# Kernel tuning notes

Hardware: AMD Instinct MI355X
Metric: run time of the kernel (lower is better)

Reference implementation:

```python
import jax, jax.numpy as jnp
import numpy as np

EPS = 1e-5  # BatchNorm eps


def _conv3x3(x, w, b):
    # x: [B,C,H,W], w: [O,C,3,3], b: [O]
    y = jax.lax.conv_general_dilated(
        x, w, window_strides=(1, 1), padding=((1, 1), (1, 1)),
        dimension_numbers=("NCHW", "OIHW", "NCHW"))
    return y + b[None, :, None, None]


def _bilinear_gather(x, py, px):
    """Bilinear sample x at fractional coords (zero outside bounds).
    x: [B,C,H,W]; py, px: [B,K,H,W] -> returns [B,C,K,H,W]."""
    B, C, H, W = x.shape
    K = py.shape[1]
    x_flat = x.reshape(B, C, H * W)
    y0 = jnp.floor(py)
    x0 = jnp.floor(px)
    wy1 = py - y0
    wx1 = px - x0
    wy0 = 1.0 - wy1
    wx0 = 1.0 - wx1

    def gather(yi, xi):
        valid = (yi >= 0) & (yi <= H - 1) & (xi >= 0) & (xi <= W - 1)
        yc = jnp.clip(yi, 0, H - 1).astype(jnp.int32)
        xc = jnp.clip(xi, 0, W - 1).astype(jnp.int32)
        idx = (yc * W + xc).reshape(B, 1, K * H * W)
        g = jnp.take_along_axis(x_flat, idx, axis=2).reshape(B, C, K, H, W)
        return g * valid.astype(x.dtype)[:, None]

    val = (gather(y0, x0) * (wy0 * wx0)[:, None]
           + gather(y0, x0 + 1.0) * (wy0 * wx1)[:, None]
           + gather(y0 + 1.0, x0) * (wy1 * wx0)[:, None]
           + gather(y0 + 1.0, x0 + 1.0) * (wy1 * wx1)[:, None])
    return val


def _deform_conv_bn_relu(x, w_off, b_off, w_dcn, b_dcn, gamma, beta):
    B, Ci, H, W = x.shape
    Co = w_dcn.shape[0]
    # offset/mask branch: 27 = 9 dy | 9 dx (cat, then interpreted interleaved) | 9 mask
    om = _conv3x3(x, w_off, b_off)                       # [B,27,H,W]
    offset = jnp.concatenate([om[:, :9], om[:, 9:18]], axis=1)  # [B,18,H,W]
    mask = jax.nn.sigmoid(om[:, 18:27])                  # [B,9,H,W]
    dy = offset[:, 0::2]                                 # [B,9,H,W]
    dx = offset[:, 1::2]                                 # [B,9,H,W]
    # base sampling grid: stride 1, pad 1, dilation 1, 3x3 kernel
    ky = jnp.repeat(jnp.arange(3, dtype=x.dtype), 3)     # [9]
    kx = jnp.tile(jnp.arange(3, dtype=x.dtype), 3)       # [9]
    hh = jnp.arange(H, dtype=x.dtype)
    ww = jnp.arange(W, dtype=x.dtype)
    py = dy + (hh - 1.0)[None, None, :, None] + ky[None, :, None, None]
    px = dx + (ww - 1.0)[None, None, None, :] + kx[None, :, None, None]
    sampled = _bilinear_gather(x, py, px)                # [B,Ci,9,H,W]
    sampled = sampled * mask[:, None]                    # modulated (DCNv2)
    out = jnp.einsum('bckhw,ock->bohw', sampled, w_dcn.reshape(Co, Ci, 9))
    out = out + b_dcn[None, :, None, None]
    # BatchNorm2d (training mode: batch statistics, biased variance) + ReLU
    mean = jnp.mean(out, axis=(0, 2, 3), keepdims=True)
    var = jnp.mean(jnp.square(out - mean), axis=(0, 2, 3), keepdims=True)
    bn = (out - mean) * jax.lax.rsqrt(var + EPS)
    bn = bn * gamma[None, :, None, None] + beta[None, :, None, None]
    return jax.nn.relu(bn)


def setup_inputs() -> dict:
    key = jax.random.key(0)
    k0, k1, k2 = jax.random.split(key, 3)
    B, Ci, Co, H, W = 2, 256, 256, 96, 96
    x = jax.random.normal(k0, (B, Ci, H, W), jnp.float32)
    # small offset-conv weights -> offsets within a few pixels (realistic after training)
    w_off = jax.random.normal(k1, (27, Ci, 3, 3), jnp.float32) * 0.01
    b_off = jnp.zeros((27,), jnp.float32)
    w_dcn = jax.random.normal(k2, (Co, Ci, 3, 3), jnp.float32) * (1.0 / np.sqrt(Ci * 9))
    b_dcn = jnp.zeros((Co,), jnp.float32)
    gamma = jnp.ones((Co,), jnp.float32)
    beta = jnp.zeros((Co,), jnp.float32)
    return {"x": x, "w_off": w_off, "b_off": b_off, "w_dcn": w_dcn,
            "b_dcn": b_dcn, "gamma": gamma, "beta": beta}


def reference(x, w_off, b_off, w_dcn, b_dcn, gamma, beta):
    return _deform_conv_bn_relu(x, w_off, b_off, w_dcn, b_dcn, gamma, beta)
```

## Files before the change

### kernel.cpp

```cpp
#include <hip/hip_runtime.h>


typedef unsigned short ushort_t;
typedef unsigned int uint_t;
typedef __attribute__((ext_vector_type(8))) short bf16x8;
typedef __attribute__((ext_vector_type(4))) float f32x4;
typedef __attribute__((ext_vector_type(2))) float f32x2v;

#define HH 96
#define WW 96
#define HWSZ 9216
#define CI 256
#define CO 256
#define NB 2
#define NPIX 18432
#define KTOT 2304

__device__ __forceinline__ ushort_t f2bf(float f) {
  unsigned int u = __float_as_uint(f);
  u += 0x7fffu + ((u >> 16) & 1u);
  return (ushort_t)(u >> 16);
}
__device__ __forceinline__ float u2f(uint_t u) { return __uint_as_float(u); }

__device__ __forceinline__ void gload16(const void* g, void* l) {
  __builtin_amdgcn_global_load_lds(
      (const __attribute__((address_space(1))) unsigned int*)g,
      (__attribute__((address_space(3))) unsigned int*)l, 16, 0, 0);
}

__global__ void cvt_w9(const float* __restrict__ w, ushort_t* __restrict__ o) {
  int i = blockIdx.x * 256 + threadIdx.x;
  int oo = i / KTOT;
  int kk = i - oo * KTOT;
  o[(kk >> 3) * 2048 + oo * 8 + (kk & 7)] = f2bf(w[i]);
}

__global__ void cvt_woff9(const float* __restrict__ w, ushort_t* __restrict__ o) {
  int i = blockIdx.x * 256 + threadIdx.x;
  int m = i / KTOT;
  int kk = i - m * KTOT;
  float v = (m < 27) ? w[m * KTOT + kk] : 0.f;
  o[(kk >> 3) * 256 + m * 8 + (kk & 7)] = f2bf(v);
}

__global__ __launch_bounds__(512, 2) void off_gemm(
    const float* __restrict__ x, const ushort_t* __restrict__ w27r,
    float* __restrict__ om_part) {
  __shared__ __align__(16) ushort_t A27[2][2048];
  __shared__ __align__(16) ushort_t B64[4096];
  __shared__ uint2 tbl[9][64];

  const int tid = threadIdx.x;
  const int lane = tid & 63, wid = tid >> 6;
  const int p0 = blockIdx.x * 64;
  const int part = blockIdx.y;
  const int bimg = p0 / HWSZ;
  const int hw0 = p0 - bimg * HWSZ;
  const float* xb = x + (size_t)bimg * CI * HWSZ;

  for (int e = tid; e < 576; e += 512) {
    int k = e >> 6, px = e & 63;
    int hw = hw0 + px, h = hw / WW, w_ = hw - h * WW;
    int dy = k / 3 - 1, dx = k % 3 - 1;
    bool ok = (h + dy >= 0) && (h + dy < HH) && (w_ + dx >= 0) && (w_ + dx < WW);
    tbl[k][px] = make_uint2(ok ? (uint_t)(hw + dy * WW + dx) : 0u,
                            ok ? 0x3f800000u : 0u);
  }

  const int lg = lane >> 4, lm = lane & 15;
  const int wr = wid >> 2, wc = wid & 3;
  f32x4 acc = (f32x4){0.f, 0.f, 0.f, 0.f};

  int cj[8], kj[8];
#pragma unroll
  for (int j = 0; j < 8; ++j) {
    int kk = part * 1152 + wid * 8 + j;
    cj[j] = kk / 9;
    kj[j] = kk - 9 * cj[j];
  }
  __syncthreads();

  float rv0[8], rm0[8], rv1[8], rm1[8];
  const int k0 = part * 18;

#define OG_RAW(RV, RM)                                                        \
  { _Pragma("unroll") for (int j = 0; j < 8; ++j) {                           \
      uint2 e_ = tbl[kj[j]][lane];                                            \
      RV[j] = xb[cj[j] * HWSZ + (int)e_.x];                                   \
      RM[j] = u2f(e_.y);                                                      \
      kj[j] += 1; cj[j] += 7;                                                 \
      if (kj[j] == 9) { kj[j] = 0; cj[j] += 1; } } }
#define OG_GA(CH, BUF)                                                        \
  gload16(w27r + (size_t)(CH) * 2048 + (tid & 255) * 8, &A27[BUF][(wid & 3) * 512]);
#define OG_STEP(CUR, RVC, RMC, RVN, RMN, KO)                                  \
  {                                                                           \
    if ((KO) < 17) {                                                          \
      OG_RAW(RVN, RMN)                                                        \
      OG_GA(k0 + (KO) + 1, (CUR) ^ 1)                                         \
      asm volatile("s_waitcnt vmcnt(10)" ::: "memory");                       \
    } else {                                                                  \
      asm volatile("s_waitcnt vmcnt(1)" ::: "memory");                        \
    }                                                                         \
    __builtin_amdgcn_sched_barrier(0);                                        \
    {                                                                         \
      ushort_t sv_[8] __attribute__((aligned(16)));                           \
      _Pragma("unroll") for (int j = 0; j < 8; ++j)                           \
        sv_[j] = f2bf(RVC[j] * RMC[j]);                                       \
      *(uint4*)&B64[tid * 8] = *(const uint4*)sv_;                            \
    }                                                                         \
    if ((KO) < 17) asm volatile("s_waitcnt vmcnt(9) lgkmcnt(0)" ::: "memory"); \
    else           asm volatile("s_waitcnt vmcnt(0) lgkmcnt(0)" ::: "memory"); \
    __builtin_amdgcn_s_barrier();                                             \
    __builtin_amdgcn_sched_barrier(0);                                        \
    _Pragma("unroll") for (int s = 0; s < 2; ++s) {                           \
      bf16x8 af = *(const bf16x8*)&A27[CUR][((s * 4 + lg) * 32 + wr * 16 + lm) * 8]; \
      bf16x8 bfv = *(const bf16x8*)&B64[((s * 4 + lg) * 64 + wc * 16 + lm) * 8];     \
      acc = __builtin_amdgcn_mfma_f32_16x16x32_bf16(af, bfv, acc, 0, 0, 0);   \
    }                                                                         \
    asm volatile("s_waitcnt lgkmcnt(0)" ::: "memory");                        \
    __builtin_amdgcn_s_barrier();                                             \
    __builtin_amdgcn_sched_barrier(0);                                        \
  }

  OG_RAW(rv0, rm0)
  OG_GA(k0, 0)
  for (int ko2 = 0; ko2 < 9; ++ko2) {
    const int ko = ko2 * 2;
    OG_STEP(0, rv0, rm0, rv1, rm1, ko)
    OG_STEP(1, rv1, rm1, rv0, rm0, ko + 1)
  }
#undef OG_RAW
#undef OG_GA
#undef OG_STEP

  int row = wr * 16 + lg * 4;
  int col = p0 + wc * 16 + lm;
#pragma unroll
  for (int r = 0; r < 4; ++r)
    if (row + r < 27)
      om_part[((size_t)(part * 27 + row + r)) * NPIX + col] = acc[r];
}

__global__ void prep_kernel(const float* __restrict__ om_part, const float* __restrict__ b_off,
                            uint_t* __restrict__ offs, float4* __restrict__ wts) {
  int n = blockIdx.x * 128 + threadIdx.x;
  float omv[27];
#pragma unroll
  for (int ch = 0; ch < 27; ++ch)
    omv[ch] = b_off[ch] + om_part[(size_t)ch * NPIX + n] +
              om_part[((size_t)(27 + ch)) * NPIX + n];
  int hw = n % HWSZ;
  int h = hw / WW, w = hw - h * WW;
#pragma unroll
  for (int k = 0; k < 9; ++k) {
    float dy = omv[2 * k], dx = omv[2 * k + 1];
    float mk = 1.f / (1.f + __expf(-omv[18 + k]));
    float py = dy + (float)(h - 1 + k / 3);
    float px = dx + (float)(w - 1 + k % 3);
    float y0f = floorf(py), x0f = floorf(px);
    int y0 = (int)y0f, x0 = (int)x0f;
    float wy1 = py - y0f, wx1 = px - x0f;
    float wy0 = 1.f - wy1, wx0 = 1.f - wx1;
    float vy0 = (y0 >= 0 && y0 <= HH - 1) ? 1.f : 0.f;
    float vy1 = (y0 + 1 >= 0 && y0 + 1 <= HH - 1) ? 1.f : 0.f;
    int yc0 = min(max(y0, 0), HH - 1), yc1 = min(max(y0 + 1, 0), HH - 1);
    int xa = min(max(x0, 0), WW - 2);
    float a_, b_;
    if (x0 >= 0 && x0 <= WW - 2)      { a_ = wx0; b_ = wx1; }
    else if (x0 == -1)                { a_ = wx1; b_ = 0.f; }
    else if (x0 == WW - 1)            { a_ = 0.f; b_ = wx0; }
    else                              { a_ = 0.f; b_ = 0.f; }
    float s0 = mk * vy0 * wy0, s1 = mk * vy1 * wy1;
    offs[(size_t)k * NPIX + n] = (uint_t)(yc0 * WW + xa) | ((uint_t)(yc1 * WW + xa) << 16);
    wts[(size_t)k * NPIX + n] = make_float4(a_ * s0, b_ * s0, a_ * s1, b_ * s1);
  }
}

__global__ __launch_bounds__(512, 2) void sample_lds(
    const float* __restrict__ x, const uint_t* __restrict__ offs,
    const float4* __restrict__ wts, ushort_t* __restrict__ S_g) {
  __shared__ __align__(8) uint_t xp[HWSZ];
  const int tid = threadIdx.x;
  const int img = blockIdx.x >> 1;
  const int half = blockIdx.x & 1;
  const int cp = blockIdx.y;
  const int n0 = img * HWSZ + half * 4608;

  {
    const float* s0 = x + ((size_t)(img * CI + 2 * cp)) * HWSZ;
    const float* s1 = s0 + HWSZ;
#pragma unroll
    for (int i = 0; i < 9; ++i) {
      int col = i * 1024 + tid * 2;
      f32x2v c0 = *(const f32x2v*)(s0 + col);
      f32x2v c1 = *(const f32x2v*)(s1 + col);
      uint2 pk;
      pk.x = (uint_t)f2bf(c0[0]) | ((uint_t)f2bf(c1[0]) << 16);
      pk.y = (uint_t)f2bf(c0[1]) | ((uint_t)f2bf(c1[1]) << 16);
      *(uint2*)&xp[col] = pk;
    }
  }
  __syncthreads();

  for (int j = 0; j < 9; ++j) {
    const int n = n0 + tid + j * 512;
    uint_t ofr[9]; float4 wtr[9];
#pragma unroll
    for (int k = 0; k < 9; ++k) {
      ofr[k] = offs[(size_t)k * NPIX + n];
      wtr[k] = wts[(size_t)k * NPIX + n];
    }
    uint_t pkw[9];
#pragma unroll
    for (int i = 0; i < 9; ++i) pkw[i] = 0u;
#pragma unroll
    for (int k = 0; k < 9; ++k) {
      const int o0 = (int)(ofr[k] & 0xffffu);
      const int o1 = (int)(ofr[k] >> 16);
      uint_t a0 = xp[o0], a1 = xp[o0 + 1];
      uint_t b0 = xp[o1], b1 = xp[o1 + 1];
      float v0 = wtr[k].x * u2f(a0 << 16) + wtr[k].y * u2f(a1 << 16) +
                 wtr[k].z * u2f(b0 << 16) + wtr[k].w * u2f(b1 << 16);
      float v1 = wtr[k].x * u2f(a0 & 0xffff0000u) + wtr[k].y * u2f(a1 & 0xffff0000u) +
                 wtr[k].z * u2f(b0 & 0xffff0000u) + wtr[k].w * u2f(b1 & 0xffff0000u);
      const int q0 = k, q1 = 9 + k;
      pkw[q0 >> 1] |= ((uint_t)f2bf(v0)) << ((q0 & 1) * 16);
      pkw[q1 >> 1] |= ((uint_t)f2bf(v1)) << ((q1 & 1) * 16);
    }
#pragma unroll
    for (int jj = 0; jj < 9; ++jj) {
      const int kk = cp * 18 + 2 * jj;
      *(uint_t*)&S_g[((size_t)(kk >> 3) * NPIX + n) * 8 + (kk & 7)] = pkw[jj];
    }
  }
}

__global__ __launch_bounds__(512, 2) void s_gemm(
    const ushort_t* __restrict__ w9r, const ushort_t* __restrict__ S_g,
    const float* __restrict__ b_dcn, float* __restrict__ out,
    float2* __restrict__ bnp2) {
  __shared__ __align__(16) ushort_t A[4][4096];
  __shared__ __align__(16) ushort_t S[4][4096];

  const int tid = threadIdx.x;
  const int lane = tid & 63, wid = tid >> 6;
  const int p0 = blockIdx.x * 128;
  const int m0 = blockIdx.y * 128;
  const int bimg = p0 / HWSZ;
  const int hw0 = p0 - bimg * HWSZ;
  const int lg = lane >> 4, lm = lane & 15;
  const int wr = wid >> 1, wc = wid & 1;
  const int sg = tid >> 7, sp = tid & 127;

  f32x4 acc[2][4];
#pragma unroll
  for (int i = 0; i < 2; ++i)
#pragma unroll
    for (int j = 0; j < 4; ++j) acc[i][j] = (f32x4){0.f, 0.f, 0.f, 0.f};

#define SG_STAGE(CH, BUF)                                                     \
  {                                                                           \
    gload16(w9r + ((size_t)((CH) * 4 + sg) * 256 + m0 + sp) * 8,              \
            &A[BUF][(sg * 128 + sp) * 8]);                                    \
    gload16(S_g + ((size_t)((CH) * 4 + sg) * NPIX + p0 + sp) * 8,             \
            &S[BUF][(sg * 128 + sp) * 8]);                                    \
  }
#define SG_MFMA(BUF)                                                         \
  {                                                                          \
    bf16x8 af0 = *(const bf16x8*)&A[BUF][(lg * 128 + wr * 32 + lm) * 8];     \
    bf16x8 af1 = *(const bf16x8*)&A[BUF][(lg * 128 + wr * 32 + 16 + lm) * 8];\
    _Pragma("unroll") for (int ni = 0; ni < 4; ++ni) {                       \
      bf16x8 bfv = *(const bf16x8*)&S[BUF][(lg * 128 + wc * 64 + ni * 16 + lm) * 8]; \
      acc[0][ni] = __builtin_amdgcn_mfma_f32_16x16x32_bf16(af0, bfv, acc[0][ni], 0, 0, 0); \
      acc[1][ni] = __builtin_amdgcn_mfma_f32_16x16x32_bf16(af1, bfv, acc[1][ni], 0, 0, 0); \
    }                                                                        \
  }

  SG_STAGE(0, 0)
  SG_STAGE(1, 1)
  for (int ko = 0; ko < 72; ++ko) {
    if (ko < 70) {
      SG_STAGE(ko + 2, (ko + 2) & 3)
      asm volatile("s_waitcnt vmcnt(4)" ::: "memory");
    } else if (ko == 70) {
      asm volatile("s_waitcnt vmcnt(2)" ::: "memory");
    } else {
      asm volatile("s_waitcnt vmcnt(0)" ::: "memory");
    }
    __builtin_amdgcn_s_barrier();
    __builtin_amdgcn_sched_barrier(0);
    SG_MFMA(ko & 3)
  }
#undef SG_STAGE
#undef SG_MFMA

  float bsum[8], bsq[8];
#pragma unroll
  for (int mi = 0; mi < 2; ++mi) {
#pragma unroll
    for (int r = 0; r < 4; ++r) {
      int o = m0 + wr * 32 + mi * 16 + lg * 4 + r;
      float b = b_dcn[o];
      float s = 0.f, q = 0.f;
#pragma unroll
      for (int ni = 0; ni < 4; ++ni) {
        float v = acc[mi][ni][r] + b;
        out[((size_t)(bimg * CO + o)) * HWSZ + hw0 + wc * 64 + ni * 16 + lm] = v;
        s += v; q += v * v;
      }
      bsum[mi * 4 + r] = s;
      bsq[mi * 4 + r] = q;
    }
  }
#pragma unroll
  for (int d = 1; d < 16; d <<= 1) {
#pragma unroll
    for (int i = 0; i < 8; ++i) {
      bsum[i] += __shfl_xor(bsum[i], d);
      bsq[i] += __shfl_xor(bsq[i], d);
    }
  }
  asm volatile("s_waitcnt lgkmcnt(0)" ::: "memory");
  __builtin_amdgcn_s_barrier();
  float* red = (float*)&A[0][0];
  if (lm == 0) {
#pragma unroll
    for (int i = 0; i < 8; ++i) {
      int ol = wr * 32 + (i >> 2) * 16 + lg * 4 + (i & 3);
      red[ol * 2 + wc] = bsum[i];
      red[256 + ol * 2 + wc] = bsq[i];
    }
  }
  __syncthreads();
  if (tid < 128) {
    float s = red[tid * 2] + red[tid * 2 + 1];
    float q = red[256 + tid * 2] + red[256 + tid * 2 + 1];
    bnp2[(size_t)(m0 + tid) * 144 + blockIdx.x] = make_float2(s, q);
  }
}

__global__ __launch_bounds__(64) void bn_finl(const float2* __restrict__ bnp2,
                                              const float* __restrict__ gamma,
                                              const float* __restrict__ beta,
                                              float* __restrict__ ss) {
  int o = blockIdx.x, t = threadIdx.x;
  float s = 0.f, q = 0.f;
  for (int j = t; j < 144; j += 64) {
    float2 p = bnp2[(size_t)o * 144 + j];
    s += p.x; q += p.y;
  }
#pragma unroll
  for (int d = 32; d > 0; d >>= 1) {
    s += __shfl_xor(s, d);
    q += __shfl_xor(q, d);
  }
  if (t == 0) {
    float mean = s * (1.f / (float)NPIX);
    float var = q * (1.f / (float)NPIX) - mean * mean;
    float rstd = rsqrtf(var + 1e-5f);
    float sc = rstd * gamma[o];
    ss[o] = sc;
    ss[CO + o] = beta[o] - mean * sc;
  }
}

__global__ void bn_apply(float* __restrict__ out, const float* __restrict__ ss) {
  int i = blockIdx.x * 256 + threadIdx.x;
  float4 v = ((float4*)out)[i];
  int o = (i / (HWSZ / 4)) & 255;
  float sc = ss[o], sh = ss[CO + o];
  v.x = fmaxf(v.x * sc + sh, 0.f);
  v.y = fmaxf(v.y * sc + sh, 0.f);
  v.z = fmaxf(v.z * sc + sh, 0.f);
  v.w = fmaxf(v.w * sc + sh, 0.f);
  ((float4*)out)[i] = v;
}

extern "C" void kernel_launch(void* const* d_in, const int* in_sizes, int n_in,
                              void* d_out, int out_size, void* d_ws, size_t ws_size,
                              hipStream_t stream) {
  const float* x = (const float*)d_in[0];
  const float* w_off = (const float*)d_in[1];
  const float* b_off = (const float*)d_in[2];
  const float* w_dcn = (const float*)d_in[3];
  const float* b_dcn = (const float*)d_in[4];
  const float* gamma = (const float*)d_in[5];
  const float* beta = (const float*)d_in[6];
  float* out = (float*)d_out;

  char* ws = (char*)d_ws;

  size_t base = 84934656;
  ushort_t* S_g   = (ushort_t*)(ws);
  float*    om    = (float*)(ws + base);
  float2*   bnp2  = (float2*)(ws + base);
  uint_t*   offs  = (uint_t*)(ws + base + 3981312);
  float4*   wts   = (float4*)(ws + base + 4644864);
  ushort_t* w9r   = (ushort_t*)(ws + base + 7299072);
  ushort_t* w27r  = (ushort_t*)(ws + base + 8478720);
  float*    ss    = (float*)(ws + base + 8626176);

  cvt_w9<<<(CO * KTOT) / 256, 256, 0, stream>>>(w_dcn, w9r);
  cvt_woff9<<<(32 * KTOT) / 256, 256, 0, stream>>>(w_off, w27r);
  off_gemm<<<dim3(NPIX / 64, 2), 512, 0, stream>>>(x, w27r, om);
  prep_kernel<<<NPIX / 128, 128, 0, stream>>>(om, b_off, offs, wts);
  sample_lds<<<dim3(4, 128), 512, 0, stream>>>(x, offs, wts, S_g);
  s_gemm<<<dim3(NPIX / 128, 2), 512, 0, stream>>>(w9r, S_g, b_dcn, out, bnp2);
  bn_finl<<<CO, 64, 0, stream>>>(bnp2, gamma, beta, ss);
  bn_apply<<<(out_size / 4) / 256, 256, 0, stream>>>(out, ss);
}
```

Baseline: 144.3 us.

## Sample eight channels per block to amortize offset/weight loads and widen stores

The deformable sampling kernel now stages eight channels of the image (as packed bf16 in two LDS planes) per block instead of two, and each block handles a quarter image rather than a half. Each thread's per-pixel offset and bilinear weight loads are thereby reused across eight channels, cutting redundant global reads of offs/wts by four times, and outputs are written as full 16-byte stores aligned to the K-major layout. The cost is 144KB of LDS per block, which forces one block per CU, plus a much larger register footprint (36 packed words) and a partially idle final iteration.

```diff
diff --git a/kernel.cpp b/kernel.cpp
--- a/kernel.cpp
+++ b/kernel.cpp
@@ -16,12 +16,14 @@
 #define NPIX 18432
 #define KTOT 2304
 
-__device__ __forceinline__ ushort_t f2bf(float f) {
+__device__ __forceinline__ uint_t f2bf(float f) {
   unsigned int u = __float_as_uint(f);
   u += 0x7fffu + ((u >> 16) & 1u);
-  return (ushort_t)(u >> 16);
+  return u >> 16;
 }
 __device__ __forceinline__ float u2f(uint_t u) { return __uint_as_float(u); }
+__device__ __forceinline__ float bflo(uint_t u) { return __uint_as_float(u << 16); }
+__device__ __forceinline__ float bfhi(uint_t u) { return __uint_as_float(u & 0xffff0000u); }
 
 __device__ __forceinline__ void gload16(const void* g, void* l) {
   __builtin_amdgcn_global_load_lds(
@@ -33,7 +35,7 @@
   int i = blockIdx.x * 256 + threadIdx.x;
   int oo = i / KTOT;
   int kk = i - oo * KTOT;
-  o[(kk >> 3) * 2048 + oo * 8 + (kk & 7)] = f2bf(w[i]);
+  o[(kk >> 3) * 2048 + oo * 8 + (kk & 7)] = (ushort_t)f2bf(w[i]);
 }
 
 __global__ void cvt_woff9(const float* __restrict__ w, ushort_t* __restrict__ o) {
@@ -41,7 +43,7 @@
   int m = i / KTOT;
   int kk = i - m * KTOT;
   float v = (m < 27) ? w[m * KTOT + kk] : 0.f;
-  o[(kk >> 3) * 256 + m * 8 + (kk & 7)] = f2bf(v);
+  o[(kk >> 3) * 256 + m * 8 + (kk & 7)] = (ushort_t)f2bf(v);
 }
 
 __global__ __launch_bounds__(512, 2) void off_gemm(
@@ -106,7 +108,7 @@
     {                                                                         \
       ushort_t sv_[8] __attribute__((aligned(16)));                           \
       _Pragma("unroll") for (int j = 0; j < 8; ++j)                           \
-        sv_[j] = f2bf(RVC[j] * RMC[j]);                                       \
+        sv_[j] = (ushort_t)f2bf(RVC[j] * RMC[j]);                             \
       *(uint4*)&B64[tid * 8] = *(const uint4*)sv_;                            \
     }                                                                         \
     if ((KO) < 17) asm volatile("s_waitcnt vmcnt(9) lgkmcnt(0)" ::: "memory"); \
@@ -177,61 +179,91 @@
   }
 }
 
-__global__ __launch_bounds__(512, 2) void sample_lds(
+__global__ __launch_bounds__(512, 1) void sample8(
     const float* __restrict__ x, const uint_t* __restrict__ offs,
     const float4* __restrict__ wts, ushort_t* __restrict__ S_g) {
-  __shared__ __align__(8) uint_t xp[HWSZ];
+  __shared__ __align__(16) uint_t xqA[HWSZ * 2];
+  __shared__ __align__(16) uint_t xqB[HWSZ * 2];
   const int tid = threadIdx.x;
-  const int img = blockIdx.x >> 1;
-  const int half = blockIdx.x & 1;
-  const int cp = blockIdx.y;
-  const int n0 = img * HWSZ + half * 4608;
+  const int img = blockIdx.x >> 2;
+  const int quarter = blockIdx.x & 3;
+  const int by = blockIdx.y;
+  const int n0 = img * HWSZ + quarter * 2304;
+  const int c8 = by * 8;
 
   {
-    const float* s0 = x + ((size_t)(img * CI + 2 * cp)) * HWSZ;
-    const float* s1 = s0 + HWSZ;
+    const float* s0 = x + ((size_t)(img * CI + c8)) * HWSZ;
 #pragma unroll
     for (int i = 0; i < 9; ++i) {
       int col = i * 1024 + tid * 2;
-      f32x2v c0 = *(const f32x2v*)(s0 + col);
-      f32x2v c1 = *(const f32x2v*)(s1 + col);
-      uint2 pk;
-      pk.x = (uint_t)f2bf(c0[0]) | ((uint_t)f2bf(c1[0]) << 16);
-      pk.y = (uint_t)f2bf(c0[1]) | ((uint_t)f2bf(c1[1]) << 16);
-      *(uint2*)&xp[col] = pk;
+      f32x2v c0 = *(const f32x2v*)(s0 + 0 * HWSZ + col);
+      f32x2v c1 = *(const f32x2v*)(s0 + 1 * HWSZ + col);
+      f32x2v c2 = *(const f32x2v*)(s0 + 2 * HWSZ + col);
+      f32x2v c3 = *(const f32x2v*)(s0 + 3 * HWSZ + col);
+      uint4 pkA;
+      pkA.x = f2bf(c0[0]) | (f2bf(c1[0]) << 16);
+      pkA.y = f2bf(c2[0]) | (f2bf(c3[0]) << 16);
+      pkA.z = f2bf(c0[1]) | (f2bf(c1[1]) << 16);
+      pkA.w = f2bf(c2[1]) | (f2bf(c3[1]) << 16);
+      *(uint4*)&xqA[col * 2] = pkA;
+      f32x2v c4 = *(const f32x2v*)(s0 + 4 * HWSZ + col);
+      f32x2v c5 = *(const f32x2v*)(s0 + 5 * HWSZ + col);
+      f32x2v c6 = *(const f32x2v*)(s0 + 6 * HWSZ + col);
+      f32x2v c7 = *(const f32x2v*)(s0 + 7 * HWSZ + col);
+      uint4 pkB;
+      pkB.x = f2bf(c4[0]) | (f2bf(c5[0]) << 16);
+      pkB.y = f2bf(c6[0]) | (f2bf(c7[0]) << 16);
+      pkB.z = f2bf(c4[1]) | (f2bf(c5[1]) << 16);
+      pkB.w = f2bf(c6[1]) | (f2bf(c7[1]) << 16);
+      *(uint4*)&xqB[col * 2] = pkB;
     }
   }
   __syncthreads();
 
-  for (int j = 0; j < 9; ++j) {
-    const int n = n0 + tid + j * 512;
+  for (int it = 0; it < 5; ++it) {
+    if (it == 4 && tid >= 256) break;
+    const int n = n0 + it * 512 + tid;
     uint_t ofr[9]; float4 wtr[9];
 #pragma unroll
     for (int k = 0; k < 9; ++k) {
       ofr[k] = offs[(size_t)k * NPIX + n];
       wtr[k] = wts[(size_t)k * NPIX + n];
     }
-    uint_t pkw[9];
-#pragma unroll
-    for (int i = 0; i < 9; ++i) pkw[i] = 0u;
+    uint_t pkw[36];
+#pragma unroll
+    for (int i = 0; i < 36; ++i) pkw[i] = 0u;
 #pragma unroll
     for (int k = 0; k < 9; ++k) {
       const int o0 = (int)(ofr[k] & 0xffffu);
       const int o1 = (int)(ofr[k] >> 16);
-      uint_t a0 = xp[o0], a1 = xp[o0 + 1];
-      uint_t b0 = xp[o1], b1 = xp[o1 + 1];
-      float v0 = wtr[k].x * u2f(a0 << 16) + wtr[k].y * u2f(a1 << 16) +
-                 wtr[k].z * u2f(b0 << 16) + wtr[k].w * u2f(b1 << 16);
-      float v1 = wtr[k].x * u2f(a0 & 0xffff0000u) + wtr[k].y * u2f(a1 & 0xffff0000u) +
-                 wtr[k].z * u2f(b0 & 0xffff0000u) + wtr[k].w * u2f(b1 & 0xffff0000u);
-      const int q0 = k, q1 = 9 + k;
-      pkw[q0 >> 1] |= ((uint_t)f2bf(v0)) << ((q0 & 1) * 16);
-      pkw[q1 >> 1] |= ((uint_t)f2bf(v1)) << ((q1 & 1) * 16);
-    }
-#pragma unroll
-    for (int jj = 0; jj < 9; ++jj) {
-      const int kk = cp * 18 + 2 * jj;
-      *(uint_t*)&S_g[((size_t)(kk >> 3) * NPIX + n) * 8 + (kk & 7)] = pkw[jj];
+      const float4 wv = wtr[k];
+      uint2 A00 = *(const uint2*)&xqA[o0 * 2];
+      uint2 A01 = *(const uint2*)&xqA[o0 * 2 + 2];
+      uint2 A10 = *(const uint2*)&xqA[o1 * 2];
+      uint2 A11 = *(const uint2*)&xqA[o1 * 2 + 2];
+      uint2 B00 = *(const uint2*)&xqB[o0 * 2];
+      uint2 B01 = *(const uint2*)&xqB[o0 * 2 + 2];
+      uint2 B10 = *(const uint2*)&xqB[o1 * 2];
+      uint2 B11 = *(const uint2*)&xqB[o1 * 2 + 2];
+      float v[8];
+      v[0] = wv.x * bflo(A00.x) + wv.y * bflo(A01.x) + wv.z * bflo(A10.x) + wv.w * bflo(A11.x);
+      v[1] = wv.x * bfhi(A00.x) + wv.y * bfhi(A01.x) + wv.z * bfhi(A10.x) + wv.w * bfhi(A11.x);
+      v[2] = wv.x * bflo(A00.y) + wv.y * bflo(A01.y) + wv.z * bflo(A10.y) + wv.w * bflo(A11.y);
+      v[3] = wv.x * bfhi(A00.y) + wv.y * bfhi(A01.y) + wv.z * bfhi(A10.y) + wv.w * bfhi(A11.y);
+      v[4] = wv.x * bflo(B00.x) + wv.y * bflo(B01.x) + wv.z * bflo(B10.x) + wv.w * bflo(B11.x);
+      v[5] = wv.x * bfhi(B00.x) + wv.y * bfhi(B01.x) + wv.z * bfhi(B10.x) + wv.w * bfhi(B11.x);
+      v[6] = wv.x * bflo(B00.y) + wv.y * bflo(B01.y) + wv.z * bflo(B10.y) + wv.w * bflo(B11.y);
+      v[7] = wv.x * bfhi(B00.y) + wv.y * bfhi(B01.y) + wv.z * bfhi(B10.y) + wv.w * bfhi(B11.y);
+#pragma unroll
+      for (int c = 0; c < 8; ++c) {
+        const int q = c * 9 + k;
+        pkw[q >> 1] |= f2bf(v[c]) << ((q & 1) * 16);
+      }
+    }
+#pragma unroll
+    for (int g = 0; g < 9; ++g) {
+      uint4 st = make_uint4(pkw[4 * g], pkw[4 * g + 1], pkw[4 * g + 2], pkw[4 * g + 3]);
+      *(uint4*)&S_g[((size_t)(9 * by + g) * NPIX + n) * 8] = st;
     }
   }
 }
@@ -405,7 +437,7 @@
   cvt_woff9<<<(32 * KTOT) / 256, 256, 0, stream>>>(w_off, w27r);
   off_gemm<<<dim3(NPIX / 64, 2), 512, 0, stream>>>(x, w27r, om);
   prep_kernel<<<NPIX / 128, 128, 0, stream>>>(om, b_off, offs, wts);
-  sample_lds<<<dim3(4, 128), 512, 0, stream>>>(x, offs, wts, S_g);
+  sample8<<<dim3(8, 32), 512, 0, stream>>>(x, offs, wts, S_g);
   s_gemm<<<dim3(NPIX / 128, 2), 512, 0, stream>>>(w9r, S_g, b_dcn, out, bnp2);
   bn_finl<<<CO, 64, 0, stream>>>(bnp2, gamma, beta, ss);
   bn_apply<<<(out_size / 4) / 256, 256, 0, stream>>>(out, ss);
```

New measurement: 132.4 us. 1.09x faster.
